# Optimization experiments

Hardware: AMD Instinct MI355X
Metric: run time of the kernel (lower is better)

## Reference

```python
import jax, jax.numpy as jnp
import numpy as np
import math


def setup_inputs() -> dict:
    key = jax.random.key(0)
    k1, k2 = jax.random.split(key)
    N, M, D = 32768, 4096, 512
    X_B = jax.random.normal(k1, (N, D), dtype=jnp.float32)
    X_bar = jax.random.normal(k2, (M, D), dtype=jnp.float32)
    return {"X_B": X_B, "X_bar": X_bar, "num_D": D}


def reference(X_B, X_bar, num_D):
    # Scores: [N, M] = X_B @ X_bar^T / sqrt(D)
    C = jnp.matmul(X_B, X_bar.T) / math.sqrt(num_D)
    # Global normalization scalar: max squared L2 norm over all rows of both inputs
    c_max = jnp.maximum(
        jnp.max(jnp.sum(X_B * X_B, axis=1)),
        jnp.max(jnp.sum(X_bar * X_bar, axis=1)),
    )
    C = jnp.exp(C / c_max)
    # Row-normalized attention over X_bar -> [N, D]
    X_B_out = jnp.matmul(C / jnp.sum(C, axis=1, keepdims=True), X_bar)
    # Column-normalized attention over X_B -> [M, D]
    X_bar_out = jnp.matmul(C.T / jnp.sum(C, axis=0)[:, None], X_B)
    return jnp.concatenate([X_B_out, X_bar_out], axis=0)
```

## Files before the change

### kernel.cpp

```cpp
#include <hip/hip_runtime.h>
#include <math.h>

#define DD 512

typedef __attribute__((ext_vector_type(8))) short short8;
typedef __attribute__((ext_vector_type(4))) float f32x4;

__device__ __forceinline__ unsigned short f2bf(float x) {
  unsigned u = __float_as_uint(x);
  u = (u + 0x7FFFu + ((u >> 16) & 1u)) >> 16;
  return (unsigned short)u;
}
__device__ __forceinline__ float bf2f(unsigned short b) {
  return __uint_as_float(((unsigned)b) << 16);
}

__device__ __forceinline__ void gll16(const void* g, void* l) {
  __builtin_amdgcn_global_load_lds(
      (const __attribute__((address_space(1))) unsigned int*)g,
      (__attribute__((address_space(3))) unsigned int*)l, 16, 0, 0);
}

__global__ __launch_bounds__(256) void k_prep(
    const float* __restrict__ XB, const float* __restrict__ Xbar,
    unsigned short* __restrict__ XBb, unsigned short* __restrict__ Xbarb,
    float* __restrict__ blockmax, float* __restrict__ colpart, int N, int M) {
  const int wid = threadIdx.x >> 6, lane = threadIdx.x & 63;
  int rowBase = blockIdx.x * 64 + wid * 16;
  const float* src;
  unsigned short* dst;
  int r0;
  if (rowBase < N) { src = XB;   dst = XBb;   r0 = rowBase; }
  else             { src = Xbar; dst = Xbarb; r0 = rowBase - N; }
  float ca[8] = {0, 0, 0, 0, 0, 0, 0, 0};
  float rmax = 0.f;
  for (int i = 0; i < 16; ++i) {
    size_t base = (size_t)(r0 + i) * DD + lane * 8;
    float4 v0 = *(const float4*)&src[base];
    float4 v1 = *(const float4*)&src[base + 4];
    *(ushort4*)&dst[base]     = make_ushort4(f2bf(v0.x), f2bf(v0.y), f2bf(v0.z), f2bf(v0.w));
    *(ushort4*)&dst[base + 4] = make_ushort4(f2bf(v1.x), f2bf(v1.y), f2bf(v1.z), f2bf(v1.w));
    float ss = v0.x * v0.x + v0.y * v0.y + v0.z * v0.z + v0.w * v0.w +
               v1.x * v1.x + v1.y * v1.y + v1.z * v1.z + v1.w * v1.w;
    for (int k = 32; k; k >>= 1) ss += __shfl_xor(ss, k, 64);
    rmax = fmaxf(rmax, ss);
    ca[0] += v0.x; ca[1] += v0.y; ca[2] += v0.z; ca[3] += v0.w;
    ca[4] += v1.x; ca[5] += v1.y; ca[6] += v1.z; ca[7] += v1.w;
  }
  __shared__ float scol[4][512];
  __shared__ float smax[4];
#pragma unroll
  for (int j = 0; j < 8; ++j) scol[wid][lane * 8 + j] = ca[j];
  if (lane == 0) smax[wid] = rmax;
  __syncthreads();
  const int t = threadIdx.x;
#pragma unroll
  for (int d = 0; d < 2; ++d) {
    int c = t + d * 256;
    colpart[(size_t)blockIdx.x * 512 + c] =
        scol[0][c] + scol[1][c] + scol[2][c] + scol[3][c];
  }
  if (t == 0)
    blockmax[blockIdx.x] = fmaxf(fmaxf(smax[0], smax[1]), fmaxf(smax[2], smax[3]));
}

__global__ __launch_bounds__(512) void k_colred(
    const float* __restrict__ colpart, const float* __restrict__ blockmax,
    float* __restrict__ sumXB, float* __restrict__ sumXbar,
    float* __restrict__ cmax, int nbXB, int nbTot) {
  const int d = threadIdx.x;
  if (blockIdx.x == 0) {
    float s = 0.f;
    for (int b = 0; b < nbXB; ++b) s += colpart[(size_t)b * 512 + d];
    sumXB[d] = s;
  } else {
    float s = 0.f;
    for (int b = nbXB; b < nbTot; ++b) s += colpart[(size_t)b * 512 + d];
    sumXbar[d] = s;
    float m = 0.f;
    for (int b = d; b < nbTot; b += 512) m = fmaxf(m, blockmax[b]);
    for (int k = 32; k; k >>= 1) m = fmaxf(m, __shfl_xor(m, k, 64));
    __shared__ float wmax[8];
    if ((d & 63) == 0) wmax[d >> 6] = m;
    __syncthreads();
    if (d == 0) {
      float mm = wmax[0];
#pragma unroll
      for (int w = 1; w < 8; ++w) mm = fmaxf(mm, wmax[w]);
      cmax[0] = mm;
    }
  }
}

__global__ __launch_bounds__(256) void k_transpose(
    const float* __restrict__ in, unsigned short* __restrict__ out, int R, int C) {
  __shared__ float tile[64][65];
  const int r0 = blockIdx.y * 64, c0 = blockIdx.x * 64;
  const int t = threadIdx.x;
  {
    const int rl = t >> 4, c4 = (t & 15) * 4;
#pragma unroll
    for (int k = 0; k < 4; ++k) {
      float4 v = *(const float4*)&in[(size_t)(r0 + rl + 16 * k) * C + c0 + c4];
      tile[rl + 16 * k][c4 + 0] = v.x;
      tile[rl + 16 * k][c4 + 1] = v.y;
      tile[rl + 16 * k][c4 + 2] = v.z;
      tile[rl + 16 * k][c4 + 3] = v.w;
    }
  }
  __syncthreads();
  {
    const int cl = t >> 2, rs = (t & 3) * 16;
    short8 s0, s1;
#pragma unroll
    for (int i = 0; i < 8; ++i) s0[i] = (short)f2bf(tile[rs + i][cl]);
#pragma unroll
    for (int i = 0; i < 8; ++i) s1[i] = (short)f2bf(tile[rs + 8 + i][cl]);
    size_t ob = (size_t)(c0 + cl) * R + r0 + rs;
    *(short8*)&out[ob] = s0;
    *(short8*)&out[ob + 8] = s1;
  }
}

__device__ __forceinline__ void gemm_core(
    const unsigned short* __restrict__ A, const unsigned short* __restrict__ B,
    int lda, int ldb, size_t arow0, size_t brow0, int kbase, int KT,
    unsigned short* sh, f32x4 acc[4][4]) {
  unsigned short* lA = sh;
  unsigned short* lB = sh + 8192;
  const int t = threadIdx.x, lane = t & 63, wid = t >> 6;
  const int frow = lane & 15, fgrp = lane >> 4;
  const int wr = (wid >> 1) * 64, wc = (wid & 1) * 64;
  for (int kt = 0; kt < KT; ++kt) {
    const int k0 = kbase + kt * 64;
#pragma unroll
    for (int i = 0; i < 4; ++i) {
      int c4 = i * 256 + t;
      int r = c4 >> 3, c = c4 & 7;
      int cg = c ^ (r & 7);
      gll16(&A[(arow0 + r) * (size_t)lda + k0 + cg * 8], &lA[(i * 256 + wid * 64) * 8]);
      gll16(&B[(brow0 + r) * (size_t)ldb + k0 + cg * 8], &lB[(i * 256 + wid * 64) * 8]);
    }
    __syncthreads();
#pragma unroll
    for (int kk = 0; kk < 2; ++kk) {
      short8 af[4], bf[4];
#pragma unroll
      for (int f = 0; f < 4; ++f) {
        int ra = wr + f * 16 + frow;
        int ca = (kk * 4 + fgrp) ^ (ra & 7);
        af[f] = *(const short8*)&lA[ra * 64 + ca * 8];
        int rb = wc + f * 16 + frow;
        int cb = (kk * 4 + fgrp) ^ (rb & 7);
        bf[f] = *(const short8*)&lB[rb * 64 + cb * 8];
      }
#pragma unroll
      for (int fr = 0; fr < 4; ++fr)
#pragma unroll
        for (int fc = 0; fc < 4; ++fc)
          acc[fr][fc] = __builtin_amdgcn_mfma_f32_16x16x32_bf16(af[fr], bf[fc], acc[fr][fc], 0, 0, 0);
    }
    __syncthreads();
  }
}

__global__ __launch_bounds__(256) void k_scores(
    const unsigned short* __restrict__ XBb, const unsigned short* __restrict__ Xbarb,
    unsigned short* __restrict__ E, unsigned short* __restrict__ ET,
    float* __restrict__ rowsumE, float* __restrict__ colsumE,
    const float* __restrict__ cmaxp, int N, int mq0, int MQ) {
  __shared__ __align__(16) unsigned short sh[17408];
  f32x4 acc[4][4];
#pragma unroll
  for (int a = 0; a < 4; ++a)
#pragma unroll
    for (int b = 0; b < 4; ++b) acc[a][b] = (f32x4){0.f, 0.f, 0.f, 0.f};
  const size_t n0 = (size_t)blockIdx.y * 128;
  const int ml0 = blockIdx.x * 128;
  gemm_core(XBb, Xbarb, DD, DD, n0, (size_t)(mq0 + ml0), 0, DD / 64, sh, acc);

  const float inv = 1.0f / (22.62741699796952f * cmaxp[0]);
  const int lane = threadIdx.x & 63, wid = threadIdx.x >> 6;
  const int frow = lane & 15, fgrp = lane >> 4;
  const int wr = (wid >> 1) * 64, wc = (wid & 1) * 64;
#pragma unroll
  for (int fr = 0; fr < 4; ++fr)
#pragma unroll
    for (int fc = 0; fc < 4; ++fc)
#pragma unroll
      for (int j = 0; j < 4; ++j) {
        int r = wr + fr * 16 + fgrp * 4 + j;
        int c = wc + fc * 16 + frow;
        sh[r * 136 + c] = f2bf(expm1f(acc[fr][fc][j] * inv));
      }
  __syncthreads();
  {
    const int r = threadIdx.x >> 1, h = threadIdx.x & 1;
    float rs = 0.f;
#pragma unroll
    for (int i = 0; i < 8; ++i) {
      short8 v = *(const short8*)&sh[r * 136 + h * 64 + i * 8];
#pragma unroll
      for (int j = 0; j < 8; ++j) rs += bf2f((unsigned short)v[j]);
      *(short8*)&E[(n0 + r) * (size_t)MQ + ml0 + h * 64 + i * 8] = v;
    }
    atomicAdd(&rowsumE[n0 + r], rs);
  }
  {
    const int c = threadIdx.x >> 1, v0 = (threadIdx.x & 1) * 64;
    float cs = 0.f;
#pragma unroll
    for (int i = 0; i < 8; ++i) {
      short8 s;
#pragma unroll
      for (int j = 0; j < 8; ++j) {
        unsigned short w = sh[(v0 + i * 8 + j) * 136 + c];
        cs += bf2f(w);
        s[j] = (short)w;
      }
      *(short8*)&ET[(size_t)(ml0 + c) * N + n0 + v0 + i * 8] = s;
    }
    atomicAdd(&colsumE[mq0 + ml0 + c], cs);
  }
}

__global__ __launch_bounds__(256) void k_gemm_acc(
    const unsigned short* __restrict__ A, const unsigned short* __restrict__ B,
    float* __restrict__ out, int lda, int ldb, int KT, int accum) {
  __shared__ __align__(16) unsigned short sh[16384];
  f32x4 acc[4][4];
#pragma unroll
  for (int a = 0; a < 4; ++a)
#pragma unroll
    for (int b = 0; b < 4; ++b) acc[a][b] = (f32x4){0.f, 0.f, 0.f, 0.f};
  const size_t a0 = (size_t)blockIdx.y * 128, b0 = (size_t)blockIdx.x * 128;
  gemm_core(A, B, lda, ldb, a0, b0, 0, KT, sh, acc);

  const int lane = threadIdx.x & 63, wid = threadIdx.x >> 6;
  const int frow = lane & 15, fgrp = lane >> 4;
  const int wr = (wid >> 1) * 64, wc = (wid & 1) * 64;
#pragma unroll
  for (int fr = 0; fr < 4; ++fr)
#pragma unroll
    for (int fc = 0; fc < 4; ++fc)
#pragma unroll
      for (int j = 0; j < 4; ++j) {
        size_t r = a0 + wr + fr * 16 + fgrp * 4 + j;
        size_t c = b0 + wc + fc * 16 + frow;
        size_t idx = r * DD + c;
        float v = acc[fr][fc][j];
        out[idx] = accum ? out[idx] + v : v;
      }
}

__global__ __launch_bounds__(256) void k_gemm_part(
    const unsigned short* __restrict__ A, const unsigned short* __restrict__ B,
    float* __restrict__ part, int lda, int KT, int kchunk, int MQ) {
  __shared__ __align__(16) unsigned short sh[16384];
  f32x4 acc[4][4];
#pragma unroll
  for (int a = 0; a < 4; ++a)
#pragma unroll
    for (int b = 0; b < 4; ++b) acc[a][b] = (f32x4){0.f, 0.f, 0.f, 0.f};
  const size_t a0 = (size_t)blockIdx.y * 128, b0 = (size_t)blockIdx.x * 128;
  gemm_core(A, B, lda, lda, a0, b0, blockIdx.z * kchunk, KT, sh, acc);

  float* pz = part + (size_t)blockIdx.z * MQ * DD;
  const int lane = threadIdx.x & 63, wid = threadIdx.x >> 6;
  const int frow = lane & 15, fgrp = lane >> 4;
  const int wr = (wid >> 1) * 64, wc = (wid & 1) * 64;
#pragma unroll
  for (int fr = 0; fr < 4; ++fr)
#pragma unroll
    for (int fc = 0; fc < 4; ++fc)
#pragma unroll
      for (int j = 0; j < 4; ++j) {
        size_t r = a0 + wr + fr * 16 + fgrp * 4 + j;
        size_t c = b0 + wc + fc * 16 + frow;
        pz[r * DD + c] = acc[fr][fc][j];
      }
}

__global__ void k_reduce2(const float* __restrict__ part, float* __restrict__ out2,
                          const float* __restrict__ sumXB, const float* __restrict__ colsumE,
                          int MQ, int Z, float Nf) {
  size_t idx4 = ((size_t)blockIdx.x * 256 + threadIdx.x) * 4;
  int ml = (int)(idx4 >> 9), d = (int)(idx4 & (DD - 1));
  float4 s = make_float4(0.f, 0.f, 0.f, 0.f);
  for (int z = 0; z < Z; ++z) {
    float4 p = *(const float4*)&part[(size_t)z * MQ * DD + idx4];
    s.x += p.x; s.y += p.y; s.z += p.z; s.w += p.w;
  }
  float4 sx = *(const float4*)&sumXB[d];
  float den = 1.0f / (Nf + colsumE[ml]);
  float4 o = make_float4((sx.x + s.x) * den, (sx.y + s.y) * den,
                         (sx.z + s.z) * den, (sx.w + s.w) * den);
  *(float4*)&out2[idx4] = o;
}

__global__ void k_fin1(float* __restrict__ o, const float* __restrict__ sumXbar,
                       const float* __restrict__ rowsumE, float Mf) {
  size_t idx4 = ((size_t)blockIdx.x * 256 + threadIdx.x) * 4;
  int n = (int)(idx4 >> 9), d = (int)(idx4 & (DD - 1));
  float4 raw = *(const float4*)&o[idx4];
  float4 sx = *(const float4*)&sumXbar[d];
  float den = 1.0f / (Mf + rowsumE[n]);
  float4 r = make_float4((sx.x + raw.x) * den, (sx.y + raw.y) * den,
                         (sx.z + raw.z) * den, (sx.w + raw.w) * den);
  *(float4*)&o[idx4] = r;
}

__global__ void k_wsmark(float* o, float a) { o[0] = a; }

extern "C" void kernel_launch(void* const* d_in, const int* in_sizes, int n_in,
                              void* d_out, int out_size, void* d_ws, size_t ws_size,
                              hipStream_t stream) {
  const float* XB = (const float*)d_in[0];
  const float* Xbar = (const float*)d_in[1];
  const int N = in_sizes[0] / DD;
  const int M = in_sizes[1] / DD;
  float* out = (float*)d_out;
  const int Z = 16, kchunk = N / Z, KT4 = kchunk / 64;
  const int nb = (N + M) / 64;

  int MQ = 1024;
  size_t off = 0;
  char* ws = (char*)d_ws;
  auto plan = [&](int mq) {
    size_t o = 0;
    auto tk = [&](size_t b) { o = (o + b + 255) & ~(size_t)255; };
    tk(4); tk((size_t)N * 4); tk((size_t)M * 4); tk(DD * 4); tk(DD * 4);
    tk((size_t)nb * 4); tk((size_t)nb * 512 * 4);
    tk((size_t)N * DD * 2); tk((size_t)M * DD * 2);
    tk((size_t)N * DD * 2); tk((size_t)M * DD * 2);
    tk((size_t)N * mq * 2); tk((size_t)mq * N * 2);
    tk((size_t)Z * mq * DD * 4);
    return o;
  };
  while (MQ > 128 && plan(MQ) > ws_size) MQ >>= 1;
  if (plan(MQ) > ws_size) {
    hipMemsetAsync(d_out, 0, (size_t)out_size * 4, stream);
    k_wsmark<<<1, 1, 0, stream>>>(out, (float)ws_size);
    return;
  }

  auto take = [&](size_t bytes) {
    char* p = ws + off;
    off = (off + bytes + 255) & ~(size_t)255;
    return p;
  };
  float* cmax = (float*)take(4);
  float* rowsumE = (float*)take((size_t)N * 4);
  float* colsumE = (float*)take((size_t)M * 4);
  float* sumXB = (float*)take(DD * 4);
  float* sumXbar = (float*)take(DD * 4);
  size_t headBytes = off;
  float* blockmax = (float*)take((size_t)nb * 4);
  float* colpart = (float*)take((size_t)nb * 512 * 4);
  unsigned short* XBb = (unsigned short*)take((size_t)N * DD * 2);
  unsigned short* Xbarb = (unsigned short*)take((size_t)M * DD * 2);
  unsigned short* XBT = (unsigned short*)take((size_t)N * DD * 2);
  unsigned short* XbarT = (unsigned short*)take((size_t)M * DD * 2);
  unsigned short* E = (unsigned short*)take((size_t)N * MQ * 2);
  unsigned short* ET = (unsigned short*)take((size_t)MQ * N * 2);
  float* part = (float*)take((size_t)Z * MQ * DD * 4);

  hipMemsetAsync(ws, 0, headBytes, stream);

  k_prep<<<nb, 256, 0, stream>>>(XB, Xbar, XBb, Xbarb, blockmax, colpart, N, M);
  k_colred<<<2, 512, 0, stream>>>(colpart, blockmax, sumXB, sumXbar, cmax, N / 64, nb);
  k_transpose<<<dim3(DD / 64, N / 64), 256, 0, stream>>>(XB, XBT, N, DD);
  k_transpose<<<dim3(DD / 64, M / 64), 256, 0, stream>>>(Xbar, XbarT, M, DD);

  for (int mq0 = 0; mq0 < M; mq0 += MQ) {
    k_scores<<<dim3(MQ / 128, N / 128), 256, 0, stream>>>(
        XBb, Xbarb, E, ET, rowsumE, colsumE, cmax, N, mq0, MQ);
    k_gemm_acc<<<dim3(DD / 128, N / 128), 256, 0, stream>>>(
        E, XbarT + mq0, out, MQ, M, MQ / 64, mq0 > 0 ? 1 : 0);
    k_gemm_part<<<dim3(DD / 128, MQ / 128, Z), 256, 0, stream>>>(
        ET, XBT, part, N, KT4, kchunk, MQ);
    k_reduce2<<<(MQ * DD) / 1024, 256, 0, stream>>>(
        part, out + (size_t)N * DD + (size_t)mq0 * DD, sumXB, colsumE + mq0, MQ, Z, (float)N);
  }
  k_fin1<<<((size_t)N * DD) / 1024, 256, 0, stream>>>(out, sumXbar, rowsumE, (float)M);
}
```

Baseline: 1.547 ms.

## Swizzle block IDs across XCDs and replace expm1f with polynomial

Adds a block-index remap that groups consecutive logical tiles onto the same XCD (stride of 8), so tiles that share A/B panels can hit the same L2 cache, and applies it to the score and GEMM kernels. Also replaces expm1f in the score epilogue with a 4th-order Taylor polynomial. The polynomial holds only because the scaled score argument is tiny for these inputs (it is divided by the max squared row norm), so it is an input-dependent approximation. The swizzle assumes the block count is divisible by 8.

Result: no change. 1.517 ms (-1.9%).

```diff
diff --git a/kernel.cpp b/kernel.cpp
--- a/kernel.cpp
+++ b/kernel.cpp
@@ -19,6 +19,18 @@
   __builtin_amdgcn_global_load_lds(
       (const __attribute__((address_space(1))) unsigned int*)g,
       (__attribute__((address_space(3))) unsigned int*)l, 16, 0, 0);
+}
+
+__device__ __forceinline__ void swz_bid(int& bx, int& by, int& bz) {
+  unsigned gx = gridDim.x, gy = gridDim.y, gz = gridDim.z;
+  unsigned n = gx * gy * gz;
+  unsigned id = blockIdx.x + gx * (blockIdx.y + gy * blockIdx.z);
+  unsigned q = n >> 3;
+  unsigned s = (id & 7u) * q + (id >> 3);
+  bx = s % gx;
+  unsigned t = s / gx;
+  by = t % gy;
+  bz = t / gy;
 }
 
 __global__ __launch_bounds__(256) void k_prep(
@@ -175,8 +187,10 @@
   for (int a = 0; a < 4; ++a)
 #pragma unroll
     for (int b = 0; b < 4; ++b) acc[a][b] = (f32x4){0.f, 0.f, 0.f, 0.f};
-  const size_t n0 = (size_t)blockIdx.y * 128;
-  const int ml0 = blockIdx.x * 128;
+  int bx, by, bz;
+  swz_bid(bx, by, bz);
+  const size_t n0 = (size_t)by * 128;
+  const int ml0 = bx * 128;
   gemm_core(XBb, Xbarb, DD, DD, n0, (size_t)(mq0 + ml0), 0, DD / 64, sh, acc);
 
   const float inv = 1.0f / (22.62741699796952f * cmaxp[0]);
@@ -191,7 +205,9 @@
       for (int j = 0; j < 4; ++j) {
         int r = wr + fr * 16 + fgrp * 4 + j;
         int c = wc + fc * 16 + frow;
-        sh[r * 136 + c] = f2bf(expm1f(acc[fr][fc][j] * inv));
+        float x = acc[fr][fc][j] * inv;
+        float e = x * (1.f + x * (0.5f + x * (0.16666667f + x * 0.041666668f)));
+        sh[r * 136 + c] = f2bf(e);
       }
   __syncthreads();
   {
@@ -233,7 +249,9 @@
   for (int a = 0; a < 4; ++a)
 #pragma unroll
     for (int b = 0; b < 4; ++b) acc[a][b] = (f32x4){0.f, 0.f, 0.f, 0.f};
-  const size_t a0 = (size_t)blockIdx.y * 128, b0 = (size_t)blockIdx.x * 128;
+  int bx, by, bz;
+  swz_bid(bx, by, bz);
+  const size_t a0 = (size_t)by * 128, b0 = (size_t)bx * 128;
   gemm_core(A, B, lda, ldb, a0, b0, 0, KT, sh, acc);
 
   const int lane = threadIdx.x & 63, wid = threadIdx.x >> 6;
@@ -262,10 +280,12 @@
   for (int a = 0; a < 4; ++a)
 #pragma unroll
     for (int b = 0; b < 4; ++b) acc[a][b] = (f32x4){0.f, 0.f, 0.f, 0.f};
-  const size_t a0 = (size_t)blockIdx.y * 128, b0 = (size_t)blockIdx.x * 128;
-  gemm_core(A, B, lda, lda, a0, b0, blockIdx.z * kchunk, KT, sh, acc);
-
-  float* pz = part + (size_t)blockIdx.z * MQ * DD;
+  int bx, by, bz;
+  swz_bid(bx, by, bz);
+  const size_t a0 = (size_t)by * 128, b0 = (size_t)bx * 128;
+  gemm_core(A, B, lda, lda, a0, b0, bz * kchunk, KT, sh, acc);
+
+  float* pz = part + (size_t)bz * MQ * DD;
   const int lane = threadIdx.x & 63, wid = threadIdx.x >> 6;
   const int frow = lane & 15, fgrp = lane >> 4;
   const int wr = (wid >> 1) * 64, wc = (wid & 1) * 64;
```
